# Kernel tuning notes

Measured on AMD Instinct MI355X. Metric: run time of the kernel, lower is better.

Reference implementation:

```python
import jax, jax.numpy as jnp
import numpy as np

B = 65536   # collocation batch
D = 8       # total_dim (tokens)
H = 128     # subnet hidden_dim
E = 64      # attn_embed_dim == subnet output_dim (proj is None)
NH = 4      # attention heads
GA = 4      # groupA_size


def setup_inputs() -> dict:
    key = jax.random.key(0)
    ks = iter(jax.random.split(key, 32))
    n = lambda shape, s: jax.random.normal(next(ks), shape, dtype=jnp.float32) * s
    inp = {
        "x":  jax.random.normal(next(ks), (B, D), dtype=jnp.float32),
        "w1": n((D, H), 1.0),                 # Lin(1,H) per dim (xavier ~ sqrt(2/(1+H)))
        "b1": jnp.zeros((D, H), jnp.float32),
        "w2": n((D, H, H), 1.0 / np.sqrt(H)),
        "b2": jnp.zeros((D, H), jnp.float32),
        "w3": n((D, E, H), 1.0 / np.sqrt(H)),
        "b3": jnp.zeros((D, E), jnp.float32),
    }
    for tag in ("sa", "sb", "ca", "cb"):
        inp[f"Win_{tag}"] = n((3 * E, E), 1.0 / np.sqrt(E))
        inp[f"bin_{tag}"] = jnp.zeros((3 * E,), jnp.float32)
        inp[f"Wo_{tag}"]  = n((E, E), 1.0 / np.sqrt(E))
        inp[f"bo_{tag}"]  = jnp.zeros((E,), jnp.float32)
    inp["Wf"] = n((1, 2 * E), 1.0 / np.sqrt(2 * E))
    inp["bf"] = jnp.zeros((1,), jnp.float32)
    return inp


def _mha(q, k, v, Win, bin_, Wo, bo):
    # PyTorch nn.MultiheadAttention (batch_first=True) math
    Wq, Wk, Wv = jnp.split(Win, 3, axis=0)
    bq, bk, bv = jnp.split(bin_, 3)
    dh = E // NH
    def heads(t, W, b):
        p = t @ W.T + b                         # [B,S,E]
        return p.reshape(p.shape[0], p.shape[1], NH, dh)
    qh = heads(q, Wq, bq)
    kh = heads(k, Wk, bk)
    vh = heads(v, Wv, bv)
    att = jnp.einsum('bqhd,bkhd->bhqk', qh, kh) / jnp.sqrt(jnp.float32(dh))
    w = jax.nn.softmax(att, axis=-1)
    o = jnp.einsum('bhqk,bkhd->bqhd', w, vh)
    o = o.reshape(o.shape[0], o.shape[1], E)
    return o @ Wo.T + bo


def reference(x, w1, b1, w2, b2, w3, b3,
              Win_sa, bin_sa, Wo_sa, bo_sa,
              Win_sb, bin_sb, Wo_sb, bo_sb,
              Win_ca, bin_ca, Wo_ca, bo_ca,
              Win_cb, bin_cb, Wo_cb, bo_cb,
              Wf, bf):
    # Per-dim subnets as block-diagonal batched matmuls (activation='sin', dropout=0)
    h = jnp.sin(x[:, :, None] * w1[None] + b1[None])            # [B,D,H]
    h = jnp.sin(jnp.einsum('bdh,dkh->bdk', h, w2) + b2[None])   # [B,D,H]
    tokens = jnp.einsum('bdh,doh->bdo', h, w3) + b3[None]       # [B,D,E]

    A = tokens[:, :GA, :]
    Bt = tokens[:, GA:, :]
    A_self  = _mha(A,  A,  A,  Win_sa, bin_sa, Wo_sa, bo_sa)
    B_self  = _mha(Bt, Bt, Bt, Win_sb, bin_sb, Wo_sb, bo_sb)
    A_cross = _mha(A,  Bt, Bt, Win_ca, bin_ca, Wo_ca, bo_ca)
    B_cross = _mha(Bt, A,  A,  Win_cb, bin_cb, Wo_cb, bo_cb)

    A_pool = ((A_self + A_cross) * 0.5).mean(axis=1)            # [B,E]
    B_pool = ((B_self + B_cross) * 0.5).mean(axis=1)            # [B,E]
    combined = jnp.concatenate([A_pool, B_pool], axis=1)        # [B,2E]
    out = combined @ Wf.T + bf                                  # [B,1]
    return jax.nn.leaky_relu(out, 0.01)
```

## Files before the change

### kernel.cpp

```cpp
#include <hip/hip_runtime.h>

typedef unsigned short u16;
typedef __attribute__((ext_vector_type(8))) short short8;
typedef __attribute__((ext_vector_type(4))) short s16x4;
typedef __attribute__((ext_vector_type(4))) float f32x4;
typedef __attribute__((ext_vector_type(2))) unsigned int u32x2;

#define OFF_U     0
#define OFF_CV    1024
#define OFF_CONST 1040
#define OFF_CTAG  1044
#define OFF_BA    1056
#define OFF_BB    1328
#define OFF_WA_B    6400
#define OFF_WB_B    41216
#define OFF_W2P_B   76032
#define OFF_W3P_B   338176
#define OFF_TOK_B   469248

#define P_STRIDE 280
#define PSIDE    (32 * P_STRIDE)

static __device__ __forceinline__ u16 f2bf(float f) {
  unsigned int bits = __float_as_uint(f);
  bits += 0x7fffu + ((bits >> 16) & 1u);
  return (u16)(bits >> 16);
}
static __device__ __forceinline__ unsigned rbits(float f) {
  unsigned b = __float_as_uint(f);
  return b + 0x7fffu + ((b >> 16) & 1u);
}
static __device__ __forceinline__ float bf2f(u16 u) {
  return __uint_as_float(((unsigned int)u) << 16);
}

__global__ __launch_bounds__(64) void prep_fold(
    const float* __restrict__ win_sa, const float* __restrict__ bin_sa,
    const float* __restrict__ wo_sa,  const float* __restrict__ bo_sa,
    const float* __restrict__ win_sb, const float* __restrict__ bin_sb,
    const float* __restrict__ wo_sb,  const float* __restrict__ bo_sb,
    const float* __restrict__ win_ca, const float* __restrict__ bin_ca,
    const float* __restrict__ wo_ca,  const float* __restrict__ bo_ca,
    const float* __restrict__ win_cb, const float* __restrict__ bin_cb,
    const float* __restrict__ wo_cb,  const float* __restrict__ bo_cb,
    const float* __restrict__ Wf, float* __restrict__ ws) {
  __shared__ float v_lds[64];
  const int t = threadIdx.x;
  const int tag = blockIdx.x;
  const float* wins[4] = {win_sa, win_sb, win_ca, win_cb};
  const float* bins[4] = {bin_sa, bin_sb, bin_ca, bin_cb};
  const float* wos[4]  = {wo_sa, wo_sb, wo_ca, wo_cb};
  const float* bos[4]  = {bo_sa, bo_sb, bo_ca, bo_cb};
  const float* wfh = Wf + ((tag == 0 || tag == 2) ? 0 : 64);
  float v = 0.f;
#pragma unroll
  for (int e = 0; e < 64; e++) v += wos[tag][e * 64 + t] * wfh[e];
  v_lds[t] = v;
  __syncthreads();
#pragma unroll
  for (int h = 0; h < 4; h++) {
    float u = 0.f;
#pragma unroll
    for (int dp = 0; dp < 16; dp++)
      u += wins[tag][(128 + h * 16 + dp) * 64 + t] * v_lds[h * 16 + dp];
    ws[OFF_U + tag * 256 + h * 64 + t] = u;
  }
  if (t < 4) {
    float cv = 0.f;
#pragma unroll
    for (int dp = 0; dp < 16; dp++)
      cv += bins[tag][128 + t * 16 + dp] * v_lds[t * 16 + dp];
    ws[OFF_CV + tag * 4 + t] = cv;
  }
  if (t == 0) {
    float c = 0.f;
#pragma unroll
    for (int e = 0; e < 64; e++) c += bos[tag][e] * wfh[e];
    ws[OFF_CTAG + tag] = c;
  }
}

__global__ __launch_bounds__(256) void prep_pack(
    const float* __restrict__ w2, const float* __restrict__ w3,
    const float* __restrict__ win_sa, const float* __restrict__ win_sb,
    const float* __restrict__ win_ca, const float* __restrict__ win_cb,
    const float* __restrict__ bin_sa, const float* __restrict__ bin_sb,
    const float* __restrict__ bin_ca, const float* __restrict__ bin_cb,
    const float* __restrict__ bf,
    float* __restrict__ ws, u16* __restrict__ w2p, u16* __restrict__ w3p,
    u16* __restrict__ WA, u16* __restrict__ WB) {
  int idx = blockIdx.x * 256 + threadIdx.x;
  if (idx < 131072) {
    int d = idx >> 14, rem = idx & 16383;
    int f = rem >> 9, ks = f >> 3, nt = f & 7;
    int r2 = rem & 511, l = r2 >> 3, j = r2 & 7;
    int quad = l >> 4, m15 = l & 15;
    w2p[idx] = f2bf(w2[(d * 128 + nt * 16 + m15) * 128 + ks * 32 + quad * 8 + j]);
  } else if (idx < 196608) {
    int i = idx - 131072;
    int d = i >> 13, rem = i & 8191;
    int f = rem >> 9, ks = f >> 2, nt = f & 3;
    int r2 = rem & 511, l = r2 >> 3, j = r2 & 7;
    int quad = l >> 4, m15 = l & 15;
    w3p[i] = f2bf(w3[(d * 64 + nt * 16 + m15) * 128 + ks * 32 + quad * 8 + j]);
  } else if (idx < 214016) {
    int i = idx - 196608;
    int nt = i >> 10, rem = i & 1023;
    int half = rem >> 9, r2 = rem & 511, l = r2 >> 3, j = r2 & 7;
    int n = nt * 16 + (l & 15), k = half * 32 + (l >> 4) * 8 + j;
    float v;
    if (n < 64)       v = win_sa[n * 64 + k] * 0.25f;
    else if (n < 128) v = win_sa[n * 64 + k];
    else if (n < 192) v = win_ca[(n - 128) * 64 + k] * 0.25f;
    else if (n < 256) v = win_cb[(n - 128) * 64 + k];
    else if (n < 260) v = ws[OFF_U + 0 * 256 + (n - 256) * 64 + k];
    else if (n < 264) v = ws[OFF_U + 3 * 256 + (n - 260) * 64 + k];
    else              v = 0.f;
    WA[i] = f2bf(v);
  } else if (idx < 231424) {
    int i = idx - 214016;
    int nt = i >> 10, rem = i & 1023;
    int half = rem >> 9, r2 = rem & 511, l = r2 >> 3, j = r2 & 7;
    int n = nt * 16 + (l & 15), k = half * 32 + (l >> 4) * 8 + j;
    float v;
    if (n < 64)       v = win_sb[n * 64 + k] * 0.25f;
    else if (n < 128) v = win_sb[n * 64 + k];
    else if (n < 192) v = win_cb[(n - 128) * 64 + k] * 0.25f;
    else if (n < 256) v = win_ca[(n - 128) * 64 + k];
    else if (n < 260) v = ws[OFF_U + 1 * 256 + (n - 256) * 64 + k];
    else if (n < 264) v = ws[OFF_U + 2 * 256 + (n - 260) * 64 + k];
    else              v = 0.f;
    WB[i] = f2bf(v);
  } else if (idx < 231696) {
    int n = idx - 231424;
    float v;
    if (n < 64)       v = bin_sa[n] * 0.25f;
    else if (n < 128) v = bin_sa[n];
    else if (n < 192) v = bin_ca[n - 128] * 0.25f;
    else if (n < 256) v = bin_cb[n - 128];
    else if (n < 260) v = ws[OFF_CV + 0 * 4 + (n - 256)];
    else if (n < 264) v = ws[OFF_CV + 3 * 4 + (n - 260)];
    else              v = 0.f;
    ws[OFF_BA + n] = v;
  } else if (idx < 231968) {
    int n = idx - 231696;
    float v;
    if (n < 64)       v = bin_sb[n] * 0.25f;
    else if (n < 128) v = bin_sb[n];
    else if (n < 192) v = bin_cb[n - 128] * 0.25f;
    else if (n < 256) v = bin_ca[n - 128];
    else if (n < 260) v = ws[OFF_CV + 1 * 4 + (n - 256)];
    else if (n < 264) v = ws[OFF_CV + 2 * 4 + (n - 260)];
    else              v = 0.f;
    ws[OFF_BB + n] = v;
  } else if (idx == 231968) {
    ws[OFF_CONST] = 0.5f * (ws[OFF_CTAG] + ws[OFF_CTAG + 1] +
                            ws[OFF_CTAG + 2] + ws[OFF_CTAG + 3]) + bf[0];
  }
}

__global__ __launch_bounds__(256, 4) void tokens_kernel(
    const float* __restrict__ x, const float* __restrict__ w1,
    const float* __restrict__ b1, const float* __restrict__ b2,
    const float* __restrict__ b3, const u16* __restrict__ w2p,
    const u16* __restrict__ w3p, u16* __restrict__ tok_out) {
  __shared__ __align__(16) u16 scratch[4][16 * 136];
  const int t = threadIdx.x;
  const int wave = t >> 6, lane = t & 63;
  const int m15 = lane & 15, quad = lane >> 4;
  const int d = blockIdx.x & 7;
  const int g = blockIdx.x >> 3;
  const int b0 = g * 64 + wave * 16;
  const float xv = x[(size_t)(b0 + m15) * 8 + d];

  short8 afr[4];
#pragma unroll
  for (int ks = 0; ks < 4; ks++) {
    const float* w1p = w1 + d * 128 + ks * 32 + quad * 8;
    const float* b1p = b1 + d * 128 + ks * 32 + quad * 8;
    float4 wa = *(const float4*)w1p, wb = *(const float4*)(w1p + 4);
    float4 ba = *(const float4*)b1p, bb = *(const float4*)(b1p + 4);
    short8 a;
    a[0] = (short)f2bf(__sinf(xv * wa.x + ba.x));
    a[1] = (short)f2bf(__sinf(xv * wa.y + ba.y));
    a[2] = (short)f2bf(__sinf(xv * wa.z + ba.z));
    a[3] = (short)f2bf(__sinf(xv * wa.w + ba.w));
    a[4] = (short)f2bf(__sinf(xv * wb.x + bb.x));
    a[5] = (short)f2bf(__sinf(xv * wb.y + bb.y));
    a[6] = (short)f2bf(__sinf(xv * wb.z + bb.z));
    a[7] = (short)f2bf(__sinf(xv * wb.w + bb.w));
    afr[ks] = a;
  }
  const u16* w2base = w2p + d * 16384 + lane * 8;
  f32x4 acc2[8];
#pragma unroll
  for (int nt = 0; nt < 8; nt++) acc2[nt] = (f32x4){0.f, 0.f, 0.f, 0.f};
#pragma unroll
  for (int ks = 0; ks < 4; ks++) {
#pragma unroll
    for (int nt = 0; nt < 8; nt++) {
      short8 bfr = *(const short8*)(w2base + (ks * 8 + nt) * 512);
      acc2[nt] = __builtin_amdgcn_mfma_f32_16x16x32_bf16(afr[ks], bfr, acc2[nt], 0, 0, 0);
    }
  }
#pragma unroll
  for (int nt = 0; nt < 8; nt++) {
    float bias = b2[d * 128 + m15 + 16 * nt];
#pragma unroll
    for (int r = 0; r < 4; r++)
      scratch[wave][(quad * 4 + r) * 136 + m15 + 16 * nt] =
          f2bf(__sinf(acc2[nt][r] + bias));
  }
  const u16* w3base = w3p + d * 8192 + lane * 8;
  f32x4 acc3[4];
#pragma unroll
  for (int nt = 0; nt < 4; nt++) acc3[nt] = (f32x4){0.f, 0.f, 0.f, 0.f};
#pragma unroll
  for (int ks = 0; ks < 4; ks++) {
    short8 af = *(const short8*)(&scratch[wave][m15 * 136 + ks * 32 + quad * 8]);
#pragma unroll
    for (int nt = 0; nt < 4; nt++) {
      short8 bfr = *(const short8*)(w3base + (ks * 4 + nt) * 512);
      acc3[nt] = __builtin_amdgcn_mfma_f32_16x16x32_bf16(af, bfr, acc3[nt], 0, 0, 0);
    }
  }
#pragma unroll
  for (int nt = 0; nt < 4; nt++) {
    float bias = b3[d * 64 + m15 + 16 * nt];
#pragma unroll
    for (int r = 0; r < 4; r++)
      scratch[wave][(quad * 4 + r) * 136 + m15 + 16 * nt] = f2bf(acc3[nt][r] + bias);
  }
  {
    int chunk = lane & 7;
#pragma unroll
    for (int it = 0; it < 2; it++) {
      int row_l = (lane >> 3) + it * 8;
      short8 v = *(const short8*)&scratch[wave][row_l * 136 + chunk * 8];
      *(short8*)(tok_out + ((size_t)(d * 65536 + b0 + row_l)) * 64 + chunk * 8) = v;
    }
  }
}

__global__ __launch_bounds__(128, 4) void attn_kernel(
    const float* __restrict__ ws, const u16* __restrict__ tok,
    const u16* __restrict__ WA, const u16* __restrict__ WB,
    float* __restrict__ out) {
  __shared__ __align__(16) u16 P[2 * PSIDE];
  const int t = threadIdx.x;
  const int wave = t >> 6, lane = t & 63;
  const int m15 = lane & 15, quad = lane >> 4;
  const int side = wave;
  const int b0 = blockIdx.x * 8;
  const float cst = ws[OFF_CONST];

  {
    const u16* W = side ? WB : WA;
    const float* bias = ws + (side ? OFF_BB : OFF_BA);
    const int dd = (m15 & 3) + side * 4;
    short8 a0[2], a1[2];
#pragma unroll
    for (int mt = 0; mt < 2; mt++) {
      const int e = mt * 4 + (m15 >> 2);
      const u16* ab = tok + ((size_t)(dd * 65536 + b0 + e)) * 64 + quad * 8;
      a0[mt] = *(const short8*)ab;
      a1[mt] = *(const short8*)(ab + 32);
    }
    u16* Pb = &P[side * PSIDE];
#pragma unroll
    for (int nt = 0; nt < 17; nt++) {
      const u16* bp = W + nt * 1024 + lane * 8;
      short8 w0f = *(const short8*)bp;
      short8 w1f = *(const short8*)(bp + 512);
      float4 bi = *(const float4*)(bias + nt * 16 + quad * 4);
#pragma unroll
      for (int mt = 0; mt < 2; mt++) {
        f32x4 acc = {0.f, 0.f, 0.f, 0.f};
        acc = __builtin_amdgcn_mfma_f32_16x16x32_bf16(w0f, a0[mt], acc, 0, 0, 0);
        acc = __builtin_amdgcn_mfma_f32_16x16x32_bf16(w1f, a1[mt], acc, 0, 0, 0);
        u32x2 pk;
        pk[0] = (rbits(acc[1] + bi.y) & 0xffff0000u) | (rbits(acc[0] + bi.x) >> 16);
        pk[1] = (rbits(acc[3] + bi.w) & 0xffff0000u) | (rbits(acc[2] + bi.z) >> 16);
        *(u32x2*)&Pb[(mt * 16 + m15) * P_STRIDE + nt * 16 + quad * 4] = pk;
      }
    }
  }
  __syncthreads();
  {
    const int eg = wave;
    const int q2 = (quad & 1) * 8;
    const bool hiq = (quad & 2) != 0;
    const u16* row0 = P + (size_t)(eg * 16 + m15) * P_STRIDE;
    const u16* row1 = row0 + PSIDE;
    float acc = 0.f;
#pragma unroll
    for (int tag = 0; tag < 4; tag++) {
      const int qs = tag & 1, cross = tag >> 1;
      const int ks2 = qs ^ cross;
      const u16* rowK = ks2 ? row1 : row0;
      const u16* rowQ = qs ? row1 : row0;
      const u16* vbase = P + ks2 * PSIDE +
                         (size_t)(eg * 16 + quad * 4) * P_STRIDE + 256 + cross * 4;
      s16x4 vv0 = *(const s16x4*)(vbase);
      s16x4 vv1 = *(const s16x4*)(vbase + P_STRIDE);
      s16x4 vv2 = *(const s16x4*)(vbase + 2 * P_STRIDE);
      s16x4 vv3 = *(const s16x4*)(vbase + 3 * P_STRIDE);
#pragma unroll
      for (int h = 0; h < 4; h++) {
        const int kcol = 64 + cross * 128 + h * 16 + q2;
        const int qcol = hiq ? 264 : (cross * 128 + h * 16 + q2);
        short8 afr = *(const short8*)(rowK + kcol);
        short8 bfr = *(const short8*)(rowQ + qcol);
        f32x4 c = {0.f, 0.f, 0.f, 0.f};
        c = __builtin_amdgcn_mfma_f32_16x16x32_bf16(afr, bfr, c, 0, 0, 0);
        float e0 = __expf(c[0]), e1 = __expf(c[1]);
        float e2 = __expf(c[2]), e3 = __expf(c[3]);
        float o = e0 * bf2f((u16)vv0[h]) + e1 * bf2f((u16)vv1[h]) +
                  e2 * bf2f((u16)vv2[h]) + e3 * bf2f((u16)vv3[h]);
        acc += o * __builtin_amdgcn_rcpf(e0 + e1 + e2 + e3);
      }
    }
    acc += __shfl_xor(acc, 1);
    acc += __shfl_xor(acc, 2);
    if (quad == (m15 >> 2) && (m15 & 3) == 0) {
      float val = 0.125f * acc + cst;
      out[b0 + eg * 4 + quad] = val > 0.f ? val : 0.01f * val;
    }
  }
}

extern "C" void kernel_launch(void* const* d_in, const int* in_sizes, int n_in,
                              void* d_out, int out_size, void* d_ws, size_t ws_size,
                              hipStream_t stream) {
  const float* x      = (const float*)d_in[0];
  const float* w1     = (const float*)d_in[1];
  const float* b1     = (const float*)d_in[2];
  const float* w2     = (const float*)d_in[3];
  const float* b2     = (const float*)d_in[4];
  const float* w3     = (const float*)d_in[5];
  const float* b3     = (const float*)d_in[6];
  const float* win_sa = (const float*)d_in[7];
  const float* bin_sa = (const float*)d_in[8];
  const float* wo_sa  = (const float*)d_in[9];
  const float* bo_sa  = (const float*)d_in[10];
  const float* win_sb = (const float*)d_in[11];
  const float* bin_sb = (const float*)d_in[12];
  const float* wo_sb  = (const float*)d_in[13];
  const float* bo_sb  = (const float*)d_in[14];
  const float* win_ca = (const float*)d_in[15];
  const float* bin_ca = (const float*)d_in[16];
  const float* wo_ca  = (const float*)d_in[17];
  const float* bo_ca  = (const float*)d_in[18];
  const float* win_cb = (const float*)d_in[19];
  const float* bin_cb = (const float*)d_in[20];
  const float* wo_cb  = (const float*)d_in[21];
  const float* bo_cb  = (const float*)d_in[22];
  const float* Wf     = (const float*)d_in[23];
  const float* bf     = (const float*)d_in[24];
  float* ws = (float*)d_ws;
  u16* WAp    = (u16*)((char*)d_ws + OFF_WA_B);
  u16* WBp    = (u16*)((char*)d_ws + OFF_WB_B);
  u16* w2p    = (u16*)((char*)d_ws + OFF_W2P_B);
  u16* w3p    = (u16*)((char*)d_ws + OFF_W3P_B);
  u16* tokbuf = (u16*)((char*)d_ws + OFF_TOK_B);
  float* out = (float*)d_out;

  prep_fold<<<4, 64, 0, stream>>>(win_sa, bin_sa, wo_sa, bo_sa,
                                  win_sb, bin_sb, wo_sb, bo_sb,
                                  win_ca, bin_ca, wo_ca, bo_ca,
                                  win_cb, bin_cb, wo_cb, bo_cb,
                                  Wf, ws);
  prep_pack<<<907, 256, 0, stream>>>(w2, w3, win_sa, win_sb, win_ca, win_cb,
                                     bin_sa, bin_sb, bin_ca, bin_cb, bf,
                                     ws, w2p, w3p, WAp, WBp);
  tokens_kernel<<<8192, 256, 0, stream>>>(x, w1, b1, b2, b3, w2p, w3p, tokbuf);
  attn_kernel<<<8192, 128, 0, stream>>>(ws, tokbuf, WAp, WBp, out);
}
```

Measured before the change: 229.0 us.

## Process two M-tiles per wave in tokens kernel to reuse weight fragments

Each wave in the tokens kernel now handles 32 batch rows instead of 16, so every w2/w3 B-fragment load feeds two MFMAs, and the grid is halved. MFMA operands are swapped so the accumulator holds transposed tiles, which allows bias to be loaded as float4 and results to be packed as two bf16 pairs per 64-bit LDS store. Block indexing is reordered so consecutive blocks share the same dimension d. The cost is doubled accumulator registers and LDS scratch, which may reduce occupancy.

```diff
diff --git a/kernel.cpp b/kernel.cpp
--- a/kernel.cpp
+++ b/kernel.cpp
@@ -164,77 +164,99 @@
     const float* __restrict__ b1, const float* __restrict__ b2,
     const float* __restrict__ b3, const u16* __restrict__ w2p,
     const u16* __restrict__ w3p, u16* __restrict__ tok_out) {
-  __shared__ __align__(16) u16 scratch[4][16 * 136];
+  __shared__ __align__(16) u16 scratch[4][32 * 136];
   const int t = threadIdx.x;
   const int wave = t >> 6, lane = t & 63;
   const int m15 = lane & 15, quad = lane >> 4;
-  const int d = blockIdx.x & 7;
-  const int g = blockIdx.x >> 3;
-  const int b0 = g * 64 + wave * 16;
-  const float xv = x[(size_t)(b0 + m15) * 8 + d];
-
-  short8 afr[4];
+  const int d = blockIdx.x >> 9;
+  const int g = blockIdx.x & 511;
+  const int b0 = g * 128 + wave * 32;
+  const float xv0 = x[(size_t)(b0 + m15) * 8 + d];
+  const float xv1 = x[(size_t)(b0 + 16 + m15) * 8 + d];
+
+  const u16* w2base = w2p + d * 16384 + lane * 8;
+  f32x4 acc2[2][8];
+#pragma unroll
+  for (int mt = 0; mt < 2; mt++)
+#pragma unroll
+    for (int nt = 0; nt < 8; nt++) acc2[mt][nt] = (f32x4){0.f, 0.f, 0.f, 0.f};
 #pragma unroll
   for (int ks = 0; ks < 4; ks++) {
     const float* w1p = w1 + d * 128 + ks * 32 + quad * 8;
     const float* b1p = b1 + d * 128 + ks * 32 + quad * 8;
     float4 wa = *(const float4*)w1p, wb = *(const float4*)(w1p + 4);
     float4 ba = *(const float4*)b1p, bb = *(const float4*)(b1p + 4);
-    short8 a;
-    a[0] = (short)f2bf(__sinf(xv * wa.x + ba.x));
-    a[1] = (short)f2bf(__sinf(xv * wa.y + ba.y));
-    a[2] = (short)f2bf(__sinf(xv * wa.z + ba.z));
-    a[3] = (short)f2bf(__sinf(xv * wa.w + ba.w));
-    a[4] = (short)f2bf(__sinf(xv * wb.x + bb.x));
-    a[5] = (short)f2bf(__sinf(xv * wb.y + bb.y));
-    a[6] = (short)f2bf(__sinf(xv * wb.z + bb.z));
-    a[7] = (short)f2bf(__sinf(xv * wb.w + bb.w));
-    afr[ks] = a;
-  }
-  const u16* w2base = w2p + d * 16384 + lane * 8;
-  f32x4 acc2[8];
-#pragma unroll
-  for (int nt = 0; nt < 8; nt++) acc2[nt] = (f32x4){0.f, 0.f, 0.f, 0.f};
-#pragma unroll
-  for (int ks = 0; ks < 4; ks++) {
+    short8 a0, a1;
+    a0[0] = (short)f2bf(__sinf(xv0 * wa.x + ba.x));
+    a0[1] = (short)f2bf(__sinf(xv0 * wa.y + ba.y));
+    a0[2] = (short)f2bf(__sinf(xv0 * wa.z + ba.z));
+    a0[3] = (short)f2bf(__sinf(xv0 * wa.w + ba.w));
+    a0[4] = (short)f2bf(__sinf(xv0 * wb.x + bb.x));
+    a0[5] = (short)f2bf(__sinf(xv0 * wb.y + bb.y));
+    a0[6] = (short)f2bf(__sinf(xv0 * wb.z + bb.z));
+    a0[7] = (short)f2bf(__sinf(xv0 * wb.w + bb.w));
+    a1[0] = (short)f2bf(__sinf(xv1 * wa.x + ba.x));
+    a1[1] = (short)f2bf(__sinf(xv1 * wa.y + ba.y));
+    a1[2] = (short)f2bf(__sinf(xv1 * wa.z + ba.z));
+    a1[3] = (short)f2bf(__sinf(xv1 * wa.w + ba.w));
+    a1[4] = (short)f2bf(__sinf(xv1 * wb.x + bb.x));
+    a1[5] = (short)f2bf(__sinf(xv1 * wb.y + bb.y));
+    a1[6] = (short)f2bf(__sinf(xv1 * wb.z + bb.z));
+    a1[7] = (short)f2bf(__sinf(xv1 * wb.w + bb.w));
 #pragma unroll
     for (int nt = 0; nt < 8; nt++) {
       short8 bfr = *(const short8*)(w2base + (ks * 8 + nt) * 512);
-      acc2[nt] = __builtin_amdgcn_mfma_f32_16x16x32_bf16(afr[ks], bfr, acc2[nt], 0, 0, 0);
+      acc2[0][nt] = __builtin_amdgcn_mfma_f32_16x16x32_bf16(bfr, a0, acc2[0][nt], 0, 0, 0);
+      acc2[1][nt] = __builtin_amdgcn_mfma_f32_16x16x32_bf16(bfr, a1, acc2[1][nt], 0, 0, 0);
     }
   }
 #pragma unroll
   for (int nt = 0; nt < 8; nt++) {
-    float bias = b2[d * 128 + m15 + 16 * nt];
-#pragma unroll
-    for (int r = 0; r < 4; r++)
-      scratch[wave][(quad * 4 + r) * 136 + m15 + 16 * nt] =
-          f2bf(__sinf(acc2[nt][r] + bias));
+    float4 bi = *(const float4*)(b2 + d * 128 + nt * 16 + quad * 4);
+#pragma unroll
+    for (int mt = 0; mt < 2; mt++) {
+      u32x2 pk;
+      pk[0] = (rbits(__sinf(acc2[mt][nt][1] + bi.y)) & 0xffff0000u) |
+              (rbits(__sinf(acc2[mt][nt][0] + bi.x)) >> 16);
+      pk[1] = (rbits(__sinf(acc2[mt][nt][3] + bi.w)) & 0xffff0000u) |
+              (rbits(__sinf(acc2[mt][nt][2] + bi.z)) >> 16);
+      *(u32x2*)&scratch[wave][(mt * 16 + m15) * 136 + nt * 16 + quad * 4] = pk;
+    }
   }
   const u16* w3base = w3p + d * 8192 + lane * 8;
-  f32x4 acc3[4];
-#pragma unroll
-  for (int nt = 0; nt < 4; nt++) acc3[nt] = (f32x4){0.f, 0.f, 0.f, 0.f};
+  f32x4 acc3[2][4];
+#pragma unroll
+  for (int mt = 0; mt < 2; mt++)
+#pragma unroll
+    for (int nt = 0; nt < 4; nt++) acc3[mt][nt] = (f32x4){0.f, 0.f, 0.f, 0.f};
 #pragma unroll
   for (int ks = 0; ks < 4; ks++) {
-    short8 af = *(const short8*)(&scratch[wave][m15 * 136 + ks * 32 + quad * 8]);
+    short8 af0 = *(const short8*)&scratch[wave][m15 * 136 + ks * 32 + quad * 8];
+    short8 af1 = *(const short8*)&scratch[wave][(16 + m15) * 136 + ks * 32 + quad * 8];
 #pragma unroll
     for (int nt = 0; nt < 4; nt++) {
       short8 bfr = *(const short8*)(w3base + (ks * 4 + nt) * 512);
-      acc3[nt] = __builtin_amdgcn_mfma_f32_16x16x32_bf16(af, bfr, acc3[nt], 0, 0, 0);
+      acc3[0][nt] = __builtin_amdgcn_mfma_f32_16x16x32_bf16(bfr, af0, acc3[0][nt], 0, 0, 0);
+      acc3[1][nt] = __builtin_amdgcn_mfma_f32_16x16x32_bf16(bfr, af1, acc3[1][nt], 0, 0, 0);
     }
   }
 #pragma unroll
   for (int nt = 0; nt < 4; nt++) {
-    float bias = b3[d * 64 + m15 + 16 * nt];
-#pragma unroll
-    for (int r = 0; r < 4; r++)
-      scratch[wave][(quad * 4 + r) * 136 + m15 + 16 * nt] = f2bf(acc3[nt][r] + bias);
+    float4 bi = *(const float4*)(b3 + d * 64 + nt * 16 + quad * 4);
+#pragma unroll
+    for (int mt = 0; mt < 2; mt++) {
+      u32x2 pk;
+      pk[0] = (rbits(acc3[mt][nt][1] + bi.y) & 0xffff0000u) |
+              (rbits(acc3[mt][nt][0] + bi.x) >> 16);
+      pk[1] = (rbits(acc3[mt][nt][3] + bi.w) & 0xffff0000u) |
+              (rbits(acc3[mt][nt][2] + bi.z) >> 16);
+      *(u32x2*)&scratch[wave][(mt * 16 + m15) * 136 + nt * 16 + quad * 4] = pk;
+    }
   }
   {
     int chunk = lane & 7;
 #pragma unroll
-    for (int it = 0; it < 2; it++) {
+    for (int it = 0; it < 4; it++) {
       int row_l = (lane >> 3) + it * 8;
       short8 v = *(const short8*)&scratch[wave][row_l * 136 + chunk * 8];
       *(short8*)(tok_out + ((size_t)(d * 65536 + b0 + row_l)) * 64 + chunk * 8) = v;
@@ -373,6 +395,6 @@
   prep_pack<<<907, 256, 0, stream>>>(w2, w3, win_sa, win_sb, win_ca, win_cb,
                                      bin_sa, bin_sb, bin_ca, bin_cb, bf,
                                      ws, w2p, w3p, WAp, WBp);
-  tokens_kernel<<<8192, 256, 0, stream>>>(x, w1, b1, b2, b3, w2p, w3p, tokbuf);
+  tokens_kernel<<<4096, 256, 0, stream>>>(x, w1, b1, b2, b3, w2p, w3p, tokbuf);
   attn_kernel<<<8192, 128, 0, stream>>>(ws, tokbuf, WAp, WBp, out);
 }
```

Result: faster. 208.8 us (-8.8%).
